# Performance work log

Hardware: AMD Instinct MI355X
Metric: run time of the kernel (lower is better)

## Reference

```python
import jax, jax.numpy as jnp
import numpy as np

C = 256
CQK = C // 8  # 32

def setup_inputs() -> dict:
    key = jax.random.key(0)
    ks = jax.random.split(key, 8)
    x = jax.random.normal(ks[0], (4, C, 64, 64), dtype=jnp.float32)
    Wq = jax.random.normal(ks[1], (CQK, C), dtype=jnp.float32) * 0.02
    bq = jnp.zeros((CQK,), dtype=jnp.float32)
    Wk = jax.random.normal(ks[2], (CQK, C), dtype=jnp.float32) * 0.02
    bk = jnp.zeros((CQK,), dtype=jnp.float32)
    Wv = jax.random.normal(ks[3], (C, C), dtype=jnp.float32) * 0.02
    bv = jnp.zeros((C,), dtype=jnp.float32)
    # torch init: gamma = zeros(1); use small nonzero so backward path through attention is exercised? -> stay faithful: zeros
    gamma = jnp.zeros((1,), dtype=jnp.float32)
    return {"x": x, "Wq": Wq, "bq": bq, "Wk": Wk, "bk": bk, "Wv": Wv, "bv": bv, "gamma": gamma}


def reference(x, Wq, bq, Wk, bk, Wv, bv, gamma):
    B, Cc, H, W = x.shape
    N = H * W
    xf = x.reshape(B, Cc, N)                              # B,C,N
    # 1x1 convs == per-position matmuls
    q = jnp.einsum('bcn,dc->bnd', xf, Wq) + bq            # B,N,C/8  (proj_query permuted)
    k = jnp.einsum('bcn,dc->bdn', xf, Wk) + bk[:, None]   # B,C/8,N
    v = jnp.einsum('bcn,dc->bdn', xf, Wv) + bv[:, None]   # B,C,N
    energy = jnp.einsum('bnd,bdm->bnm', q, k)             # B,N,N
    attention = jax.nn.softmax(energy, axis=-1)           # softmax over last dim
    # out[b,c,m] = sum_n v[b,c,n] * attention[b,m,n]
    out = jnp.einsum('bcn,bmn->bcm', v, attention)
    out = out.reshape(B, Cc, H, W)
    return gamma * out + x
```

## Files before the change

### kernel.cpp

```cpp
#include <hip/hip_runtime.h>

#define B_  4
#define N_  4096
#define C_  256
#define D_  32

typedef __attribute__((ext_vector_type(8))) short bf8;
typedef __attribute__((ext_vector_type(4))) float f4;

__device__ __forceinline__ unsigned short bft(float f) {
    unsigned u = __builtin_bit_cast(unsigned, f);
    return (unsigned short)((u + 0x8000u) >> 16);
}
__device__ __forceinline__ unsigned pk2(float a, float b) {
    unsigned ua = __builtin_bit_cast(unsigned, a) + 0x8000u;
    unsigned ub = __builtin_bit_cast(unsigned, b) + 0x8000u;
    return __builtin_amdgcn_perm(ub, ua, 0x07060302u);
}

__global__ __launch_bounds__(256) void prep(
    const float* __restrict__ Wq, const float* __restrict__ Wk,
    const float* __restrict__ Wv,
    unsigned short* __restrict__ Wqkb, unsigned short* __restrict__ Wvb)
{
    int i = blockIdx.x * 256 + threadIdx.x;
    if (i < 8192)       Wqkb[i] = bft(Wq[i]);
    else if (i < 16384) Wqkb[i] = bft(Wk[i - 8192]);
    Wvb[i] = bft(Wv[i]);
}

__global__ __launch_bounds__(256) void qkv(
    const float* __restrict__ x,
    const unsigned short* __restrict__ Wqkb, const unsigned short* __restrict__ Wvb,
    const float* __restrict__ bq, const float* __restrict__ bk,
    const float* __restrict__ bv,
    unsigned short* __restrict__ qb, unsigned short* __restrict__ kb,
    unsigned short* __restrict__ vb)
{
    const int b = blockIdx.y, n0 = blockIdx.x * 32;
    const int t = threadIdx.x;
    const int lane = t & 63, w = t >> 6, c15 = lane & 15, g = lane >> 4;

    __shared__ __align__(16) unsigned short xs[32][264];

    {
        const int r = t >> 3, cg = t & 7;
        #pragma unroll
        for (int it = 0; it < 8; ++it) {
            int c = r + 32 * it;
            float4 v = *(const float4*)(x + ((size_t)(b * C_ + c)) * N_ + n0 + cg * 4);
            xs[cg * 4 + 0][c] = bft(v.x);
            xs[cg * 4 + 1][c] = bft(v.y);
            xs[cg * 4 + 2][c] = bft(v.z);
            xs[cg * 4 + 3][c] = bft(v.w);
        }
    }
    __syncthreads();

    f4 qkacc[2]; f4 vacc[2][4];
    const f4 fz = {0.f, 0.f, 0.f, 0.f};
    qkacc[0] = fz; qkacc[1] = fz;
    #pragma unroll
    for (int nt = 0; nt < 2; ++nt)
        #pragma unroll
        for (int ct = 0; ct < 4; ++ct) vacc[nt][ct] = fz;

    const unsigned short* wqk = Wqkb + (w * 16 + c15) * C_ + g * 8;
    const unsigned short* wv0 = Wvb + (w * 64 + c15) * C_ + g * 8;
    const unsigned short* xsp = &xs[c15][g * 8];

    #pragma unroll
    for (int ks = 0; ks < 8; ++ks) {
        bf8 xf0 = *(const bf8*)(xsp + ks * 32);
        bf8 xf1 = *(const bf8*)(xsp + 16 * 264 + ks * 32);
        bf8 af  = *(const bf8*)(wqk + ks * 32);
        qkacc[0] = __builtin_amdgcn_mfma_f32_16x16x32_bf16(af, xf0, qkacc[0], 0, 0, 0);
        qkacc[1] = __builtin_amdgcn_mfma_f32_16x16x32_bf16(af, xf1, qkacc[1], 0, 0, 0);
        #pragma unroll
        for (int ct = 0; ct < 4; ++ct) {
            bf8 bfv = *(const bf8*)(wv0 + ct * 16 * C_ + ks * 32);
            vacc[0][ct] = __builtin_amdgcn_mfma_f32_16x16x32_bf16(xf0, bfv, vacc[0][ct], 0, 0, 0);
            vacc[1][ct] = __builtin_amdgcn_mfma_f32_16x16x32_bf16(xf1, bfv, vacc[1][ct], 0, 0, 0);
        }
    }

    {
        float4 bias = (w < 2) ? *(const float4*)(bq + (w & 1) * 16 + 4 * g)
                              : *(const float4*)(bk + (w & 1) * 16 + 4 * g);
        float sc = (w < 2) ? 1.44269504f : 1.0f;
        unsigned short* base = (w < 2) ? qb : kb;
        int d0 = (w & 1) * 16 + 4 * g;
        #pragma unroll
        for (int nt = 0; nt < 2; ++nt) {
            int n = n0 + nt * 16 + c15;
            f4 a = qkacc[nt];
            uint2 pk;
            pk.x = pk2((a.x + bias.x) * sc, (a.y + bias.y) * sc);
            pk.y = pk2((a.z + bias.z) * sc, (a.w + bias.w) * sc);
            *(uint2*)(base + ((size_t)(b * N_ + n)) * D_ + d0) = pk;
        }
    }
    #pragma unroll
    for (int ct = 0; ct < 4; ++ct) {
        int cout = w * 64 + ct * 16 + c15;
        float bvv = bv[cout];
        #pragma unroll
        for (int nt = 0; nt < 2; ++nt) {
            f4 a = vacc[nt][ct];
            uint2 pk;
            pk.x = pk2(a.x + bvv, a.y + bvv);
            pk.y = pk2(a.z + bvv, a.w + bvv);
            *(uint2*)(vb + ((size_t)(b * C_ + cout)) * (size_t)N_ + n0 + nt * 16 + 4 * g) = pk;
        }
    }
}

__global__ __launch_bounds__(512, 4) void attn(
    const unsigned short* __restrict__ qb, const unsigned short* __restrict__ kb,
    const unsigned short* __restrict__ vb, const float* __restrict__ x,
    const float* __restrict__ gamma, float* __restrict__ out)
{
    const int bid = blockIdx.x;
    const int combo = bid & 7, mb = bid >> 3;
    const int b = combo >> 1, c0 = (combo & 1) * 128, m0 = mb * 64;
    const int t = threadIdx.x;
    const int lane = t & 63, w = t >> 6, c15 = lane & 15, g = lane >> 4;
    const int cq = w & 3, ksh = w >> 2;
    const int sw = (c15 & 7) << 4;

    __shared__ __align__(16) unsigned short Ps[2][64 * 128];
    __shared__ float l_s[8][64];
    __shared__ __align__(16) float l_tot[64];

    const f4 fz = {0.f, 0.f, 0.f, 0.f};

    bf8 qf[4];
    #pragma unroll
    for (int mi = 0; mi < 4; ++mi)
        qf[mi] = *(const bf8*)(qb + ((size_t)(b * N_ + m0 + mi * 16 + c15)) * D_ + g * 8);

    f4 acc[4][2];
    #pragma unroll
    for (int mt = 0; mt < 4; ++mt)
        #pragma unroll
        for (int ct = 0; ct < 2; ++ct) acc[mt][ct] = fz;
    float lr[4] = {0.f, 0.f, 0.f, 0.f};

    const unsigned short* vbase = vb + ((size_t)(b * C_ + c0 + cq * 32)) * (size_t)N_;
    const unsigned short* kbase = kb + (size_t)b * N_ * D_;

    bf8 kcur;
    bf8 vcur[2][2], vnxt[2][2];

    {
        bf8 kf0 = *(const bf8*)(kbase + (size_t)(w * 16 + c15) * D_ + g * 8);
        #pragma unroll
        for (int ki = 0; ki < 2; ++ki)
            #pragma unroll
            for (int ct = 0; ct < 2; ++ct)
                vcur[ki][ct] = *(const bf8*)(vbase + (size_t)(ct * 16 + c15) * N_
                                             + (ksh * 2 + ki) * 32 + g * 8);
        kcur = *(const bf8*)(kbase + (size_t)(128 + w * 16 + c15) * D_ + g * 8);
        char* pw = (char*)Ps[0];
        #pragma unroll
        for (int mi = 0; mi < 4; ++mi) {
            f4 s = __builtin_amdgcn_mfma_f32_16x16x32_bf16(kf0, qf[mi], fz, 0, 0, 0);
            float p0 = __builtin_amdgcn_exp2f(s.x);
            float p1 = __builtin_amdgcn_exp2f(s.y);
            float p2 = __builtin_amdgcn_exp2f(s.z);
            float p3 = __builtin_amdgcn_exp2f(s.w);
            lr[mi] += (p0 + p1) + (p2 + p3);
            uint2 pk; pk.x = pk2(p0, p1); pk.y = pk2(p2, p3);
            *(uint2*)(pw + (mi * 16 + c15) * 256 + ((w * 32 + 8 * g) ^ sw)) = pk;
        }
        asm volatile("s_waitcnt lgkmcnt(0)\n\ts_barrier" ::: "memory");
    }

    for (int i = 0; i < 31; ++i) {
        const int j0 = i << 7;
        char* pb = (char*)Ps[i & 1];
        char* pw = (char*)Ps[(i & 1) ^ 1];
        bf8 pf0[4];
        #pragma unroll
        for (int mt = 0; mt < 4; ++mt)
            pf0[mt] = *(const bf8*)(pb + (mt * 16 + c15) * 256 + ((ksh * 128 + 16 * g) ^ sw));
        f4 s[4];
        #pragma unroll
        for (int mi = 0; mi < 4; ++mi)
            s[mi] = __builtin_amdgcn_mfma_f32_16x16x32_bf16(kcur, qf[mi], fz, 0, 0, 0);
        #pragma unroll
        for (int mi = 0; mi < 4; ++mi) {
            acc[mi][0] = __builtin_amdgcn_mfma_f32_16x16x32_bf16(pf0[mi], vcur[0][0], acc[mi][0], 0, 0, 0);
            acc[mi][1] = __builtin_amdgcn_mfma_f32_16x16x32_bf16(pf0[mi], vcur[0][1], acc[mi][1], 0, 0, 0);
            float p0 = __builtin_amdgcn_exp2f(s[mi].x);
            float p1 = __builtin_amdgcn_exp2f(s[mi].y);
            float p2 = __builtin_amdgcn_exp2f(s[mi].z);
            float p3 = __builtin_amdgcn_exp2f(s[mi].w);
            lr[mi] += (p0 + p1) + (p2 + p3);
            uint2 pk; pk.x = pk2(p0, p1); pk.y = pk2(p2, p3);
            *(uint2*)(pw + (mi * 16 + c15) * 256 + ((w * 32 + 8 * g) ^ sw)) = pk;
        }
        {
            const int j1 = j0 + 128;
            #pragma unroll
            for (int ki = 0; ki < 2; ++ki)
                #pragma unroll
                for (int ct = 0; ct < 2; ++ct)
                    vnxt[ki][ct] = *(const bf8*)(vbase + (size_t)(ct * 16 + c15) * N_
                                                 + j1 + (ksh * 2 + ki) * 32 + g * 8);
            const int j2 = (i < 30) ? j0 + 256 : j0 + 128;
            kcur = *(const bf8*)(kbase + (size_t)(j2 + w * 16 + c15) * D_ + g * 8);
        }
        bf8 pf1[4];
        #pragma unroll
        for (int mt = 0; mt < 4; ++mt)
            pf1[mt] = *(const bf8*)(pb + (mt * 16 + c15) * 256 + ((ksh * 128 + 64 + 16 * g) ^ sw));
        #pragma unroll
        for (int mt = 0; mt < 4; ++mt)
            #pragma unroll
            for (int ct = 0; ct < 2; ++ct)
                acc[mt][ct] = __builtin_amdgcn_mfma_f32_16x16x32_bf16(pf1[mt], vcur[1][ct], acc[mt][ct], 0, 0, 0);
        #pragma unroll
        for (int ki = 0; ki < 2; ++ki)
            #pragma unroll
            for (int ct = 0; ct < 2; ++ct)
                vcur[ki][ct] = vnxt[ki][ct];
        asm volatile("s_waitcnt lgkmcnt(0)\n\ts_barrier" ::: "memory");
    }

    {
        char* pb = (char*)Ps[1];
        #pragma unroll
        for (int ki = 0; ki < 2; ++ki) {
            bf8 pf[4];
            #pragma unroll
            for (int mt = 0; mt < 4; ++mt)
                pf[mt] = *(const bf8*)(pb + (mt * 16 + c15) * 256 + ((ksh * 128 + ki * 64 + 16 * g) ^ sw));
            #pragma unroll
            for (int mt = 0; mt < 4; ++mt)
                #pragma unroll
                for (int ct = 0; ct < 2; ++ct)
                    acc[mt][ct] = __builtin_amdgcn_mfma_f32_16x16x32_bf16(pf[mt], vcur[ki][ct], acc[mt][ct], 0, 0, 0);
        }
    }

    #pragma unroll
    for (int mi = 0; mi < 4; ++mi) {
        lr[mi] += __shfl_xor(lr[mi], 16);
        lr[mi] += __shfl_xor(lr[mi], 32);
    }
    if (lane < 16) {
        #pragma unroll
        for (int mi = 0; mi < 4; ++mi) l_s[w][mi * 16 + lane] = lr[mi];
    }
    __syncthreads();

    float* accs = (float*)Ps;
    if (ksh == 1) {
        #pragma unroll
        for (int mt = 0; mt < 4; ++mt)
            #pragma unroll
            for (int ct = 0; ct < 2; ++ct)
                *(f4*)&accs[(((cq * 8 + mt * 2 + ct) * 64) + lane) * 4] = acc[mt][ct];
    }
    if (w == 0) {
        float sacc = 0.f;
        #pragma unroll
        for (int ww = 0; ww < 8; ++ww) sacc += l_s[ww][lane];
        l_tot[lane] = sacc;
    }
    __syncthreads();
    if (ksh == 0) {
        const float g0 = gamma[0];
        #pragma unroll
        for (int mt = 0; mt < 4; ++mt) {
            float4 lv = *(const float4*)&l_tot[mt * 16 + 4 * g];
            float i0 = 1.f / lv.x, i1 = 1.f / lv.y, i2 = 1.f / lv.z, i3 = 1.f / lv.w;
            #pragma unroll
            for (int ct = 0; ct < 2; ++ct) {
                f4 o = *(const f4*)&accs[(((cq * 8 + mt * 2 + ct) * 64) + lane) * 4];
                f4 a = acc[mt][ct];
                int c = c0 + cq * 32 + ct * 16 + c15;
                size_t base = ((size_t)(b * C_ + c)) * (size_t)N_ + m0 + mt * 16 + 4 * g;
                float4 xv = *(const float4*)(x + base);
                float4 r;
                r.x = g0 * ((a.x + o.x) * i0) + xv.x;
                r.y = g0 * ((a.y + o.y) * i1) + xv.y;
                r.z = g0 * ((a.z + o.z) * i2) + xv.z;
                r.w = g0 * ((a.w + o.w) * i3) + xv.w;
                *(float4*)(out + base) = r;
            }
        }
    }
}

extern "C" void kernel_launch(void* const* d_in, const int* in_sizes, int n_in,
                              void* d_out, int out_size, void* d_ws, size_t ws_size,
                              hipStream_t stream) {
    const float* x     = (const float*)d_in[0];
    const float* Wq    = (const float*)d_in[1];
    const float* bq    = (const float*)d_in[2];
    const float* Wk    = (const float*)d_in[3];
    const float* bk    = (const float*)d_in[4];
    const float* Wv    = (const float*)d_in[5];
    const float* bv    = (const float*)d_in[6];
    const float* gamma = (const float*)d_in[7];
    float* out = (float*)d_out;

    unsigned short* qb   = (unsigned short*)d_ws;
    unsigned short* kb   = qb + (size_t)B_ * N_ * D_;
    unsigned short* vb   = kb + (size_t)B_ * N_ * D_;
    unsigned short* Wqkb = vb + (size_t)B_ * C_ * N_;
    unsigned short* Wvb  = Wqkb + 64 * C_;

    prep<<<256, 256, 0, stream>>>(Wq, Wk, Wv, Wqkb, Wvb);
    qkv<<<dim3(128, 4), 256, 0, stream>>>(x, Wqkb, Wvb, bq, bk, bv, qb, kb, vb);
    attn<<<dim3(512), 512, 0, stream>>>(qb, kb, vb, x, gamma, out);
}
```

Baseline: 167.4 us.

## Ping-pong warp groups between score/exp and PV stages with padded LDS

The attention loop now splits the 8 warps into two groups that alternate roles each iteration. One group runs the P·V MFMAs over the whole 128-key tile while the other computes QK scores, exp2 and the bf16 P tile for the next iteration into the other buffer. The PV phase raises wave priority with s_setprio, and the XOR-swizzled P buffer is replaced by a row-padded (136-element) layout. The aim is to overlap exp/VALU work with matrix work across warps, at the cost of uneven per-role work and heavier per-warp PV loads.

After: 239.1 us. +42.9%, slower.

```diff
diff --git a/kernel.cpp b/kernel.cpp
--- a/kernel.cpp
+++ b/kernel.cpp
@@ -125,10 +125,9 @@
     const int b = combo >> 1, c0 = (combo & 1) * 128, m0 = mb * 64;
     const int t = threadIdx.x;
     const int lane = t & 63, w = t >> 6, c15 = lane & 15, g = lane >> 4;
-    const int cq = w & 3, ksh = w >> 2;
-    const int sw = (c15 & 7) << 4;
-
-    __shared__ __align__(16) unsigned short Ps[2][64 * 128];
+    const int u = w & 3, grp = w >> 2;
+
+    __shared__ __align__(16) unsigned short Ps[2][64][136];
     __shared__ float l_s[8][64];
     __shared__ __align__(16) float l_tot[64];
 
@@ -146,22 +145,25 @@
         for (int ct = 0; ct < 2; ++ct) acc[mt][ct] = fz;
     float lr[4] = {0.f, 0.f, 0.f, 0.f};
 
-    const unsigned short* vbase = vb + ((size_t)(b * C_ + c0 + cq * 32)) * (size_t)N_;
-    const unsigned short* kbase = kb + (size_t)b * N_ * D_;
-
-    bf8 kcur;
-    bf8 vcur[2][2], vnxt[2][2];
-
+    const unsigned short* kB = kb + (size_t)b * N_ * D_;
+    const unsigned short* vB = vb + ((size_t)(b * C_ + c0 + u * 32)) * (size_t)N_;
+
+    bf8 kfc[2];
+    bf8 vfp[2][2];
+
+    if (grp == 0) {
+        #pragma unroll
+        for (int nf = 0; nf < 2; ++nf)
+            kfc[nf] = *(const bf8*)(kB + (size_t)(128 + (2 * u + nf) * 16 + c15) * D_ + g * 8);
+    } else {
+        #pragma unroll
+        for (int ks = 0; ks < 2; ++ks)
+            #pragma unroll
+            for (int ct = 0; ct < 2; ++ct)
+                vfp[ks][ct] = *(const bf8*)(vB + (size_t)(ct * 16 + c15) * N_ + ks * 32 + g * 8);
+    }
     {
-        bf8 kf0 = *(const bf8*)(kbase + (size_t)(w * 16 + c15) * D_ + g * 8);
-        #pragma unroll
-        for (int ki = 0; ki < 2; ++ki)
-            #pragma unroll
-            for (int ct = 0; ct < 2; ++ct)
-                vcur[ki][ct] = *(const bf8*)(vbase + (size_t)(ct * 16 + c15) * N_
-                                             + (ksh * 2 + ki) * 32 + g * 8);
-        kcur = *(const bf8*)(kbase + (size_t)(128 + w * 16 + c15) * D_ + g * 8);
-        char* pw = (char*)Ps[0];
+        bf8 kf0 = *(const bf8*)(kB + (size_t)(w * 16 + c15) * D_ + g * 8);
         #pragma unroll
         for (int mi = 0; mi < 4; ++mi) {
             f4 s = __builtin_amdgcn_mfma_f32_16x16x32_bf16(kf0, qf[mi], fz, 0, 0, 0);
@@ -171,77 +173,80 @@
             float p3 = __builtin_amdgcn_exp2f(s.w);
             lr[mi] += (p0 + p1) + (p2 + p3);
             uint2 pk; pk.x = pk2(p0, p1); pk.y = pk2(p2, p3);
-            *(uint2*)(pw + (mi * 16 + c15) * 256 + ((w * 32 + 8 * g) ^ sw)) = pk;
+            *(uint2*)&Ps[0][mi * 16 + c15][w * 16 + 4 * g] = pk;
+        }
+    }
+    asm volatile("s_waitcnt lgkmcnt(0)\n\ts_barrier" ::: "memory");
+
+    for (int i = 0; i < 32; ++i) {
+        if (((grp ^ i) & 1) != 0) {
+            if (i + 2 < 32) {
+                #pragma unroll
+                for (int nf = 0; nf < 2; ++nf)
+                    kfc[nf] = *(const bf8*)(kB + (size_t)((i + 2) * 128 + (2 * u + nf) * 16 + c15) * D_ + g * 8);
+            }
+            bf8 vfl[2][2];
+            #pragma unroll
+            for (int ks = 0; ks < 2; ++ks)
+                #pragma unroll
+                for (int ct = 0; ct < 2; ++ct)
+                    vfl[ks][ct] = *(const bf8*)(vB + (size_t)(ct * 16 + c15) * N_
+                                                + i * 128 + (ks + 2) * 32 + g * 8);
+            const unsigned short (*pbR)[136] = Ps[i & 1];
+            __builtin_amdgcn_s_setprio(1);
+            #pragma unroll
+            for (int ks = 0; ks < 2; ++ks) {
+                bf8 pf[4];
+                #pragma unroll
+                for (int mt = 0; mt < 4; ++mt)
+                    pf[mt] = *(const bf8*)&pbR[mt * 16 + c15][ks * 32 + 8 * g];
+                #pragma unroll
+                for (int mt = 0; mt < 4; ++mt) {
+                    acc[mt][0] = __builtin_amdgcn_mfma_f32_16x16x32_bf16(pf[mt], vfp[ks][0], acc[mt][0], 0, 0, 0);
+                    acc[mt][1] = __builtin_amdgcn_mfma_f32_16x16x32_bf16(pf[mt], vfp[ks][1], acc[mt][1], 0, 0, 0);
+                }
+            }
+            #pragma unroll
+            for (int ks = 0; ks < 2; ++ks) {
+                bf8 pf[4];
+                #pragma unroll
+                for (int mt = 0; mt < 4; ++mt)
+                    pf[mt] = *(const bf8*)&pbR[mt * 16 + c15][(ks + 2) * 32 + 8 * g];
+                #pragma unroll
+                for (int mt = 0; mt < 4; ++mt) {
+                    acc[mt][0] = __builtin_amdgcn_mfma_f32_16x16x32_bf16(pf[mt], vfl[ks][0], acc[mt][0], 0, 0, 0);
+                    acc[mt][1] = __builtin_amdgcn_mfma_f32_16x16x32_bf16(pf[mt], vfl[ks][1], acc[mt][1], 0, 0, 0);
+                }
+            }
+            __builtin_amdgcn_s_setprio(0);
+        } else if (i < 31) {
+            const int j = i + 1;
+            #pragma unroll
+            for (int ks = 0; ks < 2; ++ks)
+                #pragma unroll
+                for (int ct = 0; ct < 2; ++ct)
+                    vfp[ks][ct] = *(const bf8*)(vB + (size_t)(ct * 16 + c15) * N_
+                                                + j * 128 + ks * 32 + g * 8);
+            unsigned short (*pbW)[136] = Ps[(i & 1) ^ 1];
+            #pragma unroll
+            for (int nf = 0; nf < 2; ++nf) {
+                f4 s[4];
+                #pragma unroll
+                for (int mi = 0; mi < 4; ++mi)
+                    s[mi] = __builtin_amdgcn_mfma_f32_16x16x32_bf16(kfc[nf], qf[mi], fz, 0, 0, 0);
+                #pragma unroll
+                for (int mi = 0; mi < 4; ++mi) {
+                    float p0 = __builtin_amdgcn_exp2f(s[mi].x);
+                    float p1 = __builtin_amdgcn_exp2f(s[mi].y);
+                    float p2 = __builtin_amdgcn_exp2f(s[mi].z);
+                    float p3 = __builtin_amdgcn_exp2f(s[mi].w);
+                    lr[mi] += (p0 + p1) + (p2 + p3);
+                    uint2 pk; pk.x = pk2(p0, p1); pk.y = pk2(p2, p3);
+                    *(uint2*)&pbW[mi * 16 + c15][(2 * u + nf) * 16 + 4 * g] = pk;
+                }
+            }
         }
         asm volatile("s_waitcnt lgkmcnt(0)\n\ts_barrier" ::: "memory");
-    }
-
-    for (int i = 0; i < 31; ++i) {
-        const int j0 = i << 7;
-        char* pb = (char*)Ps[i & 1];
-        char* pw = (char*)Ps[(i & 1) ^ 1];
-        bf8 pf0[4];
-        #pragma unroll
-        for (int mt = 0; mt < 4; ++mt)
-            pf0[mt] = *(const bf8*)(pb + (mt * 16 + c15) * 256 + ((ksh * 128 + 16 * g) ^ sw));
-        f4 s[4];
-        #pragma unroll
-        for (int mi = 0; mi < 4; ++mi)
-            s[mi] = __builtin_amdgcn_mfma_f32_16x16x32_bf16(kcur, qf[mi], fz, 0, 0, 0);
-        #pragma unroll
-        for (int mi = 0; mi < 4; ++mi) {
-            acc[mi][0] = __builtin_amdgcn_mfma_f32_16x16x32_bf16(pf0[mi], vcur[0][0], acc[mi][0], 0, 0, 0);
-            acc[mi][1] = __builtin_amdgcn_mfma_f32_16x16x32_bf16(pf0[mi], vcur[0][1], acc[mi][1], 0, 0, 0);
-            float p0 = __builtin_amdgcn_exp2f(s[mi].x);
-            float p1 = __builtin_amdgcn_exp2f(s[mi].y);
-            float p2 = __builtin_amdgcn_exp2f(s[mi].z);
-            float p3 = __builtin_amdgcn_exp2f(s[mi].w);
-            lr[mi] += (p0 + p1) + (p2 + p3);
-            uint2 pk; pk.x = pk2(p0, p1); pk.y = pk2(p2, p3);
-            *(uint2*)(pw + (mi * 16 + c15) * 256 + ((w * 32 + 8 * g) ^ sw)) = pk;
-        }
-        {
-            const int j1 = j0 + 128;
-            #pragma unroll
-            for (int ki = 0; ki < 2; ++ki)
-                #pragma unroll
-                for (int ct = 0; ct < 2; ++ct)
-                    vnxt[ki][ct] = *(const bf8*)(vbase + (size_t)(ct * 16 + c15) * N_
-                                                 + j1 + (ksh * 2 + ki) * 32 + g * 8);
-            const int j2 = (i < 30) ? j0 + 256 : j0 + 128;
-            kcur = *(const bf8*)(kbase + (size_t)(j2 + w * 16 + c15) * D_ + g * 8);
-        }
-        bf8 pf1[4];
-        #pragma unroll
-        for (int mt = 0; mt < 4; ++mt)
-            pf1[mt] = *(const bf8*)(pb + (mt * 16 + c15) * 256 + ((ksh * 128 + 64 + 16 * g) ^ sw));
-        #pragma unroll
-        for (int mt = 0; mt < 4; ++mt)
-            #pragma unroll
-            for (int ct = 0; ct < 2; ++ct)
-                acc[mt][ct] = __builtin_amdgcn_mfma_f32_16x16x32_bf16(pf1[mt], vcur[1][ct], acc[mt][ct], 0, 0, 0);
-        #pragma unroll
-        for (int ki = 0; ki < 2; ++ki)
-            #pragma unroll
-            for (int ct = 0; ct < 2; ++ct)
-                vcur[ki][ct] = vnxt[ki][ct];
-        asm volatile("s_waitcnt lgkmcnt(0)\n\ts_barrier" ::: "memory");
-    }
-
-    {
-        char* pb = (char*)Ps[1];
-        #pragma unroll
-        for (int ki = 0; ki < 2; ++ki) {
-            bf8 pf[4];
-            #pragma unroll
-            for (int mt = 0; mt < 4; ++mt)
-                pf[mt] = *(const bf8*)(pb + (mt * 16 + c15) * 256 + ((ksh * 128 + ki * 64 + 16 * g) ^ sw));
-            #pragma unroll
-            for (int mt = 0; mt < 4; ++mt)
-                #pragma unroll
-                for (int ct = 0; ct < 2; ++ct)
-                    acc[mt][ct] = __builtin_amdgcn_mfma_f32_16x16x32_bf16(pf[mt], vcur[ki][ct], acc[mt][ct], 0, 0, 0);
-        }
     }
 
     #pragma unroll
@@ -256,12 +261,12 @@
     __syncthreads();
 
     float* accs = (float*)Ps;
-    if (ksh == 1) {
+    if (grp == 1) {
         #pragma unroll
         for (int mt = 0; mt < 4; ++mt)
             #pragma unroll
             for (int ct = 0; ct < 2; ++ct)
-                *(f4*)&accs[(((cq * 8 + mt * 2 + ct) * 64) + lane) * 4] = acc[mt][ct];
+                *(f4*)&accs[(((u * 8 + mt * 2 + ct) * 64) + lane) * 4] = acc[mt][ct];
     }
     if (w == 0) {
         float sacc = 0.f;
@@ -270,7 +275,7 @@
         l_tot[lane] = sacc;
     }
     __syncthreads();
-    if (ksh == 0) {
+    if (grp == 0) {
         const float g0 = gamma[0];
         #pragma unroll
         for (int mt = 0; mt < 4; ++mt) {
@@ -278,9 +283,9 @@
             float i0 = 1.f / lv.x, i1 = 1.f / lv.y, i2 = 1.f / lv.z, i3 = 1.f / lv.w;
             #pragma unroll
             for (int ct = 0; ct < 2; ++ct) {
-                f4 o = *(const f4*)&accs[(((cq * 8 + mt * 2 + ct) * 64) + lane) * 4];
+                f4 o = *(const f4*)&accs[(((u * 8 + mt * 2 + ct) * 64) + lane) * 4];
                 f4 a = acc[mt][ct];
-                int c = c0 + cq * 32 + ct * 16 + c15;
+                int c = c0 + u * 32 + ct * 16 + c15;
                 size_t base = ((size_t)(b * C_ + c)) * (size_t)N_ + m0 + mt * 16 + 4 * g;
                 float4 xv = *(const float4*)(x + base);
                 float4 r;
```
